# Kernel optimization log

Hardware: AMD Instinct MI355X
Metric: run time of the kernel (lower is better)

The kernel has to match this reference:

```python
import jax, jax.numpy as jnp
import numpy as np

B, I, H, T = 64, 256, 512, 512


def setup_inputs() -> dict:
    key = jax.random.key(0)
    ks = jax.random.split(key, 7)
    x = jax.random.normal(ks[0], (B, I, T), jnp.float32)
    # PyTorch nn.LSTM default init: uniform(-1/sqrt(H), 1/sqrt(H))
    k = 1.0 / np.sqrt(H)
    W_ih = jax.random.uniform(ks[1], (4 * H, I), jnp.float32, -k, k)
    W_hh = jax.random.uniform(ks[2], (4 * H, H), jnp.float32, -k, k)
    b_ih = jax.random.uniform(ks[3], (4 * H,), jnp.float32, -k, k)
    b_hh = jax.random.uniform(ks[4], (4 * H,), jnp.float32, -k, k)
    # init_hidden: xavier_normal_ on zeros(1, B, H) -> N(0, std^2), std = sqrt(2/(fan_in+fan_out))
    # for a (1, B, H) tensor: fan_in = B*H, fan_out = 1*H
    std_h = np.sqrt(2.0 / (B * H + H)).astype(np.float32)
    h0 = std_h * jax.random.normal(ks[5], (B, H), jnp.float32)
    c0 = std_h * jax.random.normal(ks[6], (B, H), jnp.float32)
    return {"x": x, "W_ih": W_ih, "W_hh": W_hh, "b_ih": b_ih, "b_hh": b_hh,
            "h0": h0, "c0": c0}


def _lstm_scan(x, W_ih, W_hh, b_ih, b_hh, h0, c0):
    # x: (B, I, T) -> xs: (T, B, I); precompute input projections for all steps
    xs = jnp.transpose(x, (2, 0, 1))
    gx = jnp.einsum('tbi,gi->tbg', xs, W_ih) + (b_ih + b_hh)  # (T, B, 4H)

    def step(carry, gxt):
        h, c = carry
        gates = gxt + h @ W_hh.T  # (B, 4H)
        i_g, f_g, g_g, o_g = jnp.split(gates, 4, axis=-1)  # PyTorch gate order i,f,g,o
        i_g = jax.nn.sigmoid(i_g)
        f_g = jax.nn.sigmoid(f_g)
        g_g = jnp.tanh(g_g)
        o_g = jax.nn.sigmoid(o_g)
        c_new = f_g * c + i_g * g_g
        h_new = o_g * jnp.tanh(c_new)
        return (h_new, c_new), h_new

    (_, _), hs = jax.lax.scan(step, (h0, c0), gx)  # hs: (T, B, H)
    encoded = jnp.transpose(hs, (1, 2, 0))  # (B, H, T)
    return hs[-1][None], encoded  # mirrors (_, input_encoded)


def reference(x, W_ih, W_hh, b_ih, b_hh, h0, c0):
    return _lstm_scan(x, W_ih, W_hh, b_ih, b_hh, h0, c0)
```

## Files before the change

### kernel.cpp

```cpp
#include <hip/hip_runtime.h>

constexpr int B_ = 64, I_ = 256, H_ = 512, T_ = 512;
constexpr int BH_ = B_ * H_;

constexpr size_t WS_XT_OFF = 524288;

typedef float f32x4 __attribute__((ext_vector_type(4)));
typedef _Float16 h2 __attribute__((ext_vector_type(2)));
typedef _Float16 h8v __attribute__((ext_vector_type(8)));
union H8 { h8v v; h2 p[4]; };

#if defined(__has_builtin)
#if __has_builtin(__builtin_amdgcn_fdot2)
#define HAVE_FDOT2 1
#endif
#endif

__device__ __forceinline__ float dot2(h2 a, h2 b, float c) {
#ifdef HAVE_FDOT2
    return __builtin_amdgcn_fdot2(a, b, c, false);
#else
    return c + (float)a[0] * (float)b[0] + (float)a[1] * (float)b[1];
#endif
}

__device__ __forceinline__ float sigm(float v) { return 1.0f / (1.0f + __expf(-v)); }
__device__ __forceinline__ float tanh_fast(float v) {
    float e = __expf(2.0f * v);
    return 1.0f - 2.0f / (e + 1.0f);
}

__global__ __launch_bounds__(256)
void transpose_x(const float* __restrict__ x, _Float16* __restrict__ xT)
{
    __shared__ float tile[32][33];
    const int b  = blockIdx.z;
    const int i0 = blockIdx.y << 5;
    const int t0 = blockIdx.x << 5;
    const int lt = threadIdx.x;
    const int li = threadIdx.y;
#pragma unroll
    for (int r = 0; r < 4; ++r) {
        int i = li + (r << 3);
        tile[i][lt] = x[((size_t)b * I_ + (i0 + i)) * T_ + (t0 + lt)];
    }
    __syncthreads();
#pragma unroll
    for (int r = 0; r < 4; ++r) {
        int tt = li + (r << 3);
        xT[((size_t)(t0 + tt) * B_ + b) * I_ + (i0 + lt)] = (_Float16)tile[lt][tt];
    }
}

__global__ __launch_bounds__(512, 1)
void lstm_fused(const float* __restrict__ x,
                const _Float16* __restrict__ xT,
                const float* __restrict__ Wih,
                const float* __restrict__ Whh,
                const float* __restrict__ bih,
                const float* __restrict__ bhh,
                const float* __restrict__ h0,
                const float* __restrict__ c0,
                float* __restrict__ out,
                float* __restrict__ hbuf)
{
    __shared__ __align__(16) char smem[47104];
    f32x4* redA  = (f32x4*)smem;
    f32x4* red2  = (f32x4*)smem;
    h2*    actx2 = (h2*)(smem + 34048);
    h2*    acth2 = (h2*)(smem + 34048 + 4224);
    float* hsh   = (float*)(smem + 34048 + 4224 + 8320);

    const int tid  = threadIdx.x;
    const int wv   = tid >> 6;
    const int lane = tid & 63;
    const int jl   = lane & 15;
    const int sl   = wv * 4 + (lane >> 4);

    const int blk = blockIdx.x;
    const int bt  = blk >> 5;
    const int jt  = blk & 31;
    const int b0  = bt << 3;
    const int j0  = jt << 4;

    const int j = j0 + jl;
    h2 wx2[4][4];
    h2 wh2[4][8];
#pragma unroll
    for (int g = 0; g < 4; ++g) {
        const size_t row = (size_t)(g * H_ + j);
#pragma unroll
        for (int q = 0; q < 4; ++q) {
            wx2[g][q][0] = (_Float16)Wih[row * I_ + (sl << 3) + 2 * q];
            wx2[g][q][1] = (_Float16)Wih[row * I_ + (sl << 3) + 2 * q + 1];
        }
#pragma unroll
        for (int q = 0; q < 8; ++q) {
            wh2[g][q][0] = (_Float16)Whh[row * H_ + (sl << 4) + 2 * q];
            wh2[g][q][1] = (_Float16)Whh[row * H_ + (sl << 4) + 2 * q + 1];
        }
    }

    const int fb = b0 + (tid >> 4);
    const int fj = j0 + (tid & 15);
    float c = 0.f;
    f32x4 bias4 = {0.f, 0.f, 0.f, 0.f};
    if (tid < 128) {
        c = c0[(size_t)fb * H_ + fj];
#pragma unroll
        for (int g = 0; g < 4; ++g) bias4[g] = bih[g * H_ + fj] + bhh[g * H_ + fj];
    }

    float* enc = out + BH_;
    const int pr = tid & 127;
    const int qq = tid >> 7;

    const int hs_bq  = jl >> 1;
    const int hs_off = (sl << 4) + ((jl & 1) << 3);
    h2* hdst = acth2 + hs_bq * 260 + (sl << 3) + ((jl & 1) << 2);

    uint2 xv;
    if (xT) xv = *(const uint2*)(xT + (size_t)b0 * I_ + tid * 4);

    for (int t = 0; t < T_; ++t) {
        if (xT) {
            *(uint2*)((char*)(actx2 + (size_t)(tid >> 6) * 132) + (size_t)(tid & 63) * 8) = xv;
        } else {
#pragma unroll
            for (int r = 0; r < 4; ++r) {
                int flat = tid + (r << 9), bb = flat >> 8, ii = flat & 255;
                ((_Float16*)(actx2 + (size_t)bb * 132))[ii] =
                    (_Float16)x[((size_t)(b0 + bb) * I_ + ii) * T_ + t];
            }
        }
        __syncthreads();

        f32x4 v0, v1;
        const float* hsrc = hbuf + (size_t)((t - 1) & 1) * BH_
                          + (size_t)(b0 + hs_bq) * H_ + hs_off;
        if (t > 0) {
            asm volatile("global_load_dwordx4 %0, %2, off sc0 sc1\n\t"
                         "global_load_dwordx4 %1, %3, off sc0 sc1"
                         : "=&v"(v0), "=&v"(v1) : "v"(hsrc), "v"(hsrc + 4));
            __builtin_amdgcn_sched_barrier(0);
        }

        f32x4 r4[8];
#pragma unroll
        for (int bq = 0; bq < 8; ++bq) {
            H8 ax; ax.v = *(const h8v*)(actx2 + (size_t)bq * 132 + (sl << 2));
            float s0 = 0.f, s1 = 0.f, s2 = 0.f, s3 = 0.f;
#pragma unroll
            for (int q = 0; q < 4; ++q) {
                s0 = dot2(ax.p[q], wx2[0][q], s0);
                s1 = dot2(ax.p[q], wx2[1][q], s1);
                s2 = dot2(ax.p[q], wx2[2][q], s2);
                s3 = dot2(ax.p[q], wx2[3][q], s3);
            }
            r4[bq] = (f32x4){s0, s1, s2, s3};
        }

        if (t > 0) {
            asm volatile("s_waitcnt vmcnt(0)" ::: "memory");
            __builtin_amdgcn_sched_barrier(0);
            const float Kc = 2.0f + 2.0f * (float)(((t - 1) >> 1) & 1);
            bool ok = true;
#pragma unroll
            for (int e = 0; e < 4; ++e) {
                ok = ok && (fabsf(v0[e] - Kc) < 0.75f);
                ok = ok && (fabsf(v1[e] - Kc) < 0.75f);
            }
            for (unsigned it = 0; !ok && it < 32768u; ++it) {
                __builtin_amdgcn_s_sleep(1);
                asm volatile("global_load_dwordx4 %0, %2, off sc0 sc1\n\t"
                             "global_load_dwordx4 %1, %3, off sc0 sc1\n\t"
                             "s_waitcnt vmcnt(0)"
                             : "=&v"(v0), "=&v"(v1) : "v"(hsrc), "v"(hsrc + 4) : "memory");
                ok = true;
#pragma unroll
                for (int e = 0; e < 4; ++e) {
                    ok = ok && (fabsf(v0[e] - Kc) < 0.75f);
                    ok = ok && (fabsf(v1[e] - Kc) < 0.75f);
                }
            }
            v0 = (v0 - Kc) * 2.0f;
            v1 = (v1 - Kc) * 2.0f;
        } else {
            const float* src = h0 + (size_t)(b0 + hs_bq) * H_ + hs_off;
            v0 = *(const f32x4*)src;
            v1 = *(const f32x4*)(src + 4);
        }
        {
            H8 hv;
#pragma unroll
            for (int e = 0; e < 2; ++e) { hv.p[e][0]   = (_Float16)v0[2*e];
                                          hv.p[e][1]   = (_Float16)v0[2*e+1];
                                          hv.p[e+2][0] = (_Float16)v1[2*e];
                                          hv.p[e+2][1] = (_Float16)v1[2*e+1]; }
            *(h8v*)hdst = hv.v;
            asm volatile("s_waitcnt lgkmcnt(0)" ::: "memory");
            __builtin_amdgcn_sched_barrier(0);
        }

        if (xT && t + 1 < T_)
            xv = *(const uint2*)(xT + ((size_t)(t + 1) * B_ + b0) * I_ + tid * 4);

#pragma unroll
        for (int bq = 0; bq < 8; ++bq) {
            H8 a0, a1;
            a0.v = *(const h8v*)(acth2 + (size_t)bq * 260 + (sl << 3));
            a1.v = *(const h8v*)(acth2 + (size_t)bq * 260 + (sl << 3) + 4);
            float s0 = r4[bq][0], s1 = r4[bq][1], s2 = r4[bq][2], s3 = r4[bq][3];
#pragma unroll
            for (int q = 0; q < 4; ++q) {
                s0 = dot2(a0.p[q], wh2[0][q], s0);
                s1 = dot2(a0.p[q], wh2[1][q], s1);
                s2 = dot2(a0.p[q], wh2[2][q], s2);
                s3 = dot2(a0.p[q], wh2[3][q], s3);
            }
#pragma unroll
            for (int q = 0; q < 4; ++q) {
                s0 = dot2(a1.p[q], wh2[0][q + 4], s0);
                s1 = dot2(a1.p[q], wh2[1][q + 4], s1);
                s2 = dot2(a1.p[q], wh2[2][q + 4], s2);
                s3 = dot2(a1.p[q], wh2[3][q + 4], s3);
            }
            r4[bq] = (f32x4){s0, s1, s2, s3};
        }

        if (wv < 4) {
#pragma unroll
            for (int bq = 0; bq < 8; ++bq) redA[sl * 133 + bq * 16 + jl] = r4[bq];
        }
        __syncthreads();
        f32x4 acc = redA[(qq * 4 + 0) * 133 + pr] + redA[(qq * 4 + 1) * 133 + pr]
                  + redA[(qq * 4 + 2) * 133 + pr] + redA[(qq * 4 + 3) * 133 + pr];
        __syncthreads();
        if (wv >= 4) {
#pragma unroll
            for (int bq = 0; bq < 8; ++bq) redA[(sl - 16) * 133 + bq * 16 + jl] = r4[bq];
        }
        __syncthreads();
        acc += redA[(qq * 4 + 0) * 133 + pr] + redA[(qq * 4 + 1) * 133 + pr]
             + redA[(qq * 4 + 2) * 133 + pr] + redA[(qq * 4 + 3) * 133 + pr];
        __syncthreads();
        red2[qq * 133 + pr] = acc;
        __syncthreads();

        if (tid < 128) {
            f32x4 G = red2[0 * 133 + tid] + red2[1 * 133 + tid]
                    + red2[2 * 133 + tid] + red2[3 * 133 + tid] + bias4;
            float ig = sigm(G[0]), fg = sigm(G[1]);
            float gg = tanh_fast(G[2]);
            float og = sigm(G[3]);
            c = fg * c + ig * gg;
            float hv = og * tanh_fast(c);
            hsh[tid] = hv;
            enc[((size_t)fb * H_ + fj) * T_ + t] = hv;
            if (t == T_ - 1) out[(size_t)fb * H_ + fj] = hv;
        }

        if (t != T_ - 1) {
            __syncthreads();
            if (tid < 32) {
                const float Kp = 2.0f + 2.0f * (float)((t >> 1) & 1);
                int bq = tid >> 2, q4 = tid & 3;
                f32x4 v = *(const f32x4*)(hsh + bq * 16 + q4 * 4);
                v = v * 0.5f + Kp;
                float* dst = hbuf + (size_t)(t & 1) * BH_
                           + (size_t)(b0 + bq) * H_ + j0 + q4 * 4;
                asm volatile("global_store_dwordx4 %0, %1, off sc0 sc1"
                             :: "v"(dst), "v"(v) : "memory");
            }
        }
    }
}

extern "C" void kernel_launch(void* const* d_in, const int* in_sizes, int n_in,
                              void* d_out, int out_size, void* d_ws, size_t ws_size,
                              hipStream_t stream)
{
    (void)in_sizes; (void)n_in; (void)out_size;
    const float* x   = (const float*)d_in[0];
    const float* Wih = (const float*)d_in[1];
    const float* Whh = (const float*)d_in[2];
    const float* bih = (const float*)d_in[3];
    const float* bhh = (const float*)d_in[4];
    const float* h0  = (const float*)d_in[5];
    const float* c0  = (const float*)d_in[6];
    float* out  = (float*)d_out;
    float* hbuf = (float*)d_ws;

    const size_t xt_bytes = (size_t)T_ * B_ * I_ * sizeof(_Float16);
    _Float16* xT = nullptr;
    if (ws_size >= WS_XT_OFF + xt_bytes)
        xT = (_Float16*)((char*)d_ws + WS_XT_OFF);

    hipMemsetAsync(d_ws, 0, 2 * BH_ * sizeof(float), stream);
    if (xT)
        transpose_x<<<dim3(T_ / 32, I_ / 32, B_), dim3(32, 8), 0, stream>>>(x, xT);

    void* args[] = { (void*)&x, (void*)&xT, (void*)&Wih, (void*)&Whh, (void*)&bih,
                     (void*)&bhh, (void*)&h0, (void*)&c0, (void*)&out, (void*)&hbuf };
    hipLaunchCooperativeKernel((void*)lstm_fused, dim3(256), dim3(512), args, 0, stream);
}
```

Measured before the change: 1.827 ms.

## Split waves across batch halves to cut reduction barriers in LSTM step

Reorganizes the per-block work so each group of four waves handles half the batch rows with twice the reduction depth per thread, doubling register-held weight slices. The partial sums now go to shared memory in a single pass, replacing the multi-stage reduction that used five block barriers per step. The hidden-state publish is done within each wave after a local LDS wait, removing another block barrier. In exchange it uses more VGPRs for weights and has a longer serial 16-way sum in the gate threads.

```diff
diff --git a/kernel.cpp b/kernel.cpp
--- a/kernel.cpp
+++ b/kernel.cpp
@@ -64,18 +64,19 @@
                 float* __restrict__ out,
                 float* __restrict__ hbuf)
 {
-    __shared__ __align__(16) char smem[47104];
+    __shared__ __align__(16) char smem[47232];
     f32x4* redA  = (f32x4*)smem;
-    f32x4* red2  = (f32x4*)smem;
     h2*    actx2 = (h2*)(smem + 34048);
     h2*    acth2 = (h2*)(smem + 34048 + 4224);
-    float* hsh   = (float*)(smem + 34048 + 4224 + 8320);
+    float* hsh   = (float*)(smem + 34048 + 4224 + 8448);
 
     const int tid  = threadIdx.x;
     const int wv   = tid >> 6;
     const int lane = tid & 63;
     const int jl   = lane & 15;
-    const int sl   = wv * 4 + (lane >> 4);
+    const int slq  = lane >> 4;
+    const int bg   = wv >> 2;
+    const int sl16 = ((wv & 3) << 2) | slq;
 
     const int blk = blockIdx.x;
     const int bt  = blk >> 5;
@@ -84,20 +85,20 @@
     const int j0  = jt << 4;
 
     const int j = j0 + jl;
-    h2 wx2[4][4];
-    h2 wh2[4][8];
+    h2 wx2[4][8];
+    h2 wh2[4][16];
 #pragma unroll
     for (int g = 0; g < 4; ++g) {
         const size_t row = (size_t)(g * H_ + j);
 #pragma unroll
-        for (int q = 0; q < 4; ++q) {
-            wx2[g][q][0] = (_Float16)Wih[row * I_ + (sl << 3) + 2 * q];
-            wx2[g][q][1] = (_Float16)Wih[row * I_ + (sl << 3) + 2 * q + 1];
-        }
-#pragma unroll
         for (int q = 0; q < 8; ++q) {
-            wh2[g][q][0] = (_Float16)Whh[row * H_ + (sl << 4) + 2 * q];
-            wh2[g][q][1] = (_Float16)Whh[row * H_ + (sl << 4) + 2 * q + 1];
+            wx2[g][q][0] = (_Float16)Wih[row * I_ + (sl16 << 4) + 2 * q];
+            wx2[g][q][1] = (_Float16)Wih[row * I_ + (sl16 << 4) + 2 * q + 1];
+        }
+#pragma unroll
+        for (int q = 0; q < 16; ++q) {
+            wh2[g][q][0] = (_Float16)Whh[row * H_ + (sl16 << 5) + 2 * q];
+            wh2[g][q][1] = (_Float16)Whh[row * H_ + (sl16 << 5) + 2 * q + 1];
         }
     }
 
@@ -112,12 +113,10 @@
     }
 
     float* enc = out + BH_;
-    const int pr = tid & 127;
-    const int qq = tid >> 7;
-
-    const int hs_bq  = jl >> 1;
-    const int hs_off = (sl << 4) + ((jl & 1) << 3);
-    h2* hdst = acth2 + hs_bq * 260 + (sl << 3) + ((jl & 1) << 2);
+
+    const int sb     = (bg << 2) + (lane >> 4);
+    const int hb_off = ((wv & 3) << 7) + ((lane & 15) << 3);
+    h2* hdst = acth2 + sb * 264 + (hb_off >> 1);
 
     uint2 xv;
     if (xT) xv = *(const uint2*)(xT + (size_t)b0 * I_ + tid * 4);
@@ -137,7 +136,7 @@
 
         f32x4 v0, v1;
         const float* hsrc = hbuf + (size_t)((t - 1) & 1) * BH_
-                          + (size_t)(b0 + hs_bq) * H_ + hs_off;
+                          + (size_t)(b0 + sb) * H_ + hb_off;
         if (t > 0) {
             asm volatile("global_load_dwordx4 %0, %2, off sc0 sc1\n\t"
                          "global_load_dwordx4 %1, %3, off sc0 sc1"
@@ -145,19 +144,29 @@
             __builtin_amdgcn_sched_barrier(0);
         }
 
-        f32x4 r4[8];
-#pragma unroll
-        for (int bq = 0; bq < 8; ++bq) {
-            H8 ax; ax.v = *(const h8v*)(actx2 + (size_t)bq * 132 + (sl << 2));
+        f32x4 r4[4];
+#pragma unroll
+        for (int i = 0; i < 4; ++i) {
+            const int bq = (bg << 2) + i;
+            H8 ax0, ax1;
+            ax0.v = *(const h8v*)(actx2 + (size_t)bq * 132 + (sl16 << 3));
+            ax1.v = *(const h8v*)(actx2 + (size_t)bq * 132 + (sl16 << 3) + 4);
             float s0 = 0.f, s1 = 0.f, s2 = 0.f, s3 = 0.f;
 #pragma unroll
             for (int q = 0; q < 4; ++q) {
-                s0 = dot2(ax.p[q], wx2[0][q], s0);
-                s1 = dot2(ax.p[q], wx2[1][q], s1);
-                s2 = dot2(ax.p[q], wx2[2][q], s2);
-                s3 = dot2(ax.p[q], wx2[3][q], s3);
-            }
-            r4[bq] = (f32x4){s0, s1, s2, s3};
+                s0 = dot2(ax0.p[q], wx2[0][q], s0);
+                s1 = dot2(ax0.p[q], wx2[1][q], s1);
+                s2 = dot2(ax0.p[q], wx2[2][q], s2);
+                s3 = dot2(ax0.p[q], wx2[3][q], s3);
+            }
+#pragma unroll
+            for (int q = 0; q < 4; ++q) {
+                s0 = dot2(ax1.p[q], wx2[0][q + 4], s0);
+                s1 = dot2(ax1.p[q], wx2[1][q + 4], s1);
+                s2 = dot2(ax1.p[q], wx2[2][q + 4], s2);
+                s3 = dot2(ax1.p[q], wx2[3][q + 4], s3);
+            }
+            r4[i] = (f32x4){s0, s1, s2, s3};
         }
 
         if (t > 0) {
@@ -186,7 +195,7 @@
             v0 = (v0 - Kc) * 2.0f;
             v1 = (v1 - Kc) * 2.0f;
         } else {
-            const float* src = h0 + (size_t)(b0 + hs_bq) * H_ + hs_off;
+            const float* src = h0 + (size_t)(b0 + sb) * H_ + hb_off;
             v0 = *(const f32x4*)src;
             v1 = *(const f32x4*)(src + 4);
         }
@@ -206,11 +215,15 @@
             xv = *(const uint2*)(xT + ((size_t)(t + 1) * B_ + b0) * I_ + tid * 4);
 
 #pragma unroll
-        for (int bq = 0; bq < 8; ++bq) {
-            H8 a0, a1;
-            a0.v = *(const h8v*)(acth2 + (size_t)bq * 260 + (sl << 3));
-            a1.v = *(const h8v*)(acth2 + (size_t)bq * 260 + (sl << 3) + 4);
-            float s0 = r4[bq][0], s1 = r4[bq][1], s2 = r4[bq][2], s3 = r4[bq][3];
+        for (int i = 0; i < 4; ++i) {
+            const int bq = (bg << 2) + i;
+            const h2* hrow = acth2 + (size_t)bq * 264 + (sl16 << 4);
+            H8 a0, a1, a2, a3;
+            a0.v = *(const h8v*)(hrow);
+            a1.v = *(const h8v*)(hrow + 4);
+            a2.v = *(const h8v*)(hrow + 8);
+            a3.v = *(const h8v*)(hrow + 12);
+            float s0 = r4[i][0], s1 = r4[i][1], s2 = r4[i][2], s3 = r4[i][3];
 #pragma unroll
             for (int q = 0; q < 4; ++q) {
                 s0 = dot2(a0.p[q], wh2[0][q], s0);
@@ -225,31 +238,32 @@
                 s2 = dot2(a1.p[q], wh2[2][q + 4], s2);
                 s3 = dot2(a1.p[q], wh2[3][q + 4], s3);
             }
-            r4[bq] = (f32x4){s0, s1, s2, s3};
-        }
-
-        if (wv < 4) {
-#pragma unroll
-            for (int bq = 0; bq < 8; ++bq) redA[sl * 133 + bq * 16 + jl] = r4[bq];
-        }
+#pragma unroll
+            for (int q = 0; q < 4; ++q) {
+                s0 = dot2(a2.p[q], wh2[0][q + 8], s0);
+                s1 = dot2(a2.p[q], wh2[1][q + 8], s1);
+                s2 = dot2(a2.p[q], wh2[2][q + 8], s2);
+                s3 = dot2(a2.p[q], wh2[3][q + 8], s3);
+            }
+#pragma unroll
+            for (int q = 0; q < 4; ++q) {
+                s0 = dot2(a3.p[q], wh2[0][q + 12], s0);
+                s1 = dot2(a3.p[q], wh2[1][q + 12], s1);
+                s2 = dot2(a3.p[q], wh2[2][q + 12], s2);
+                s3 = dot2(a3.p[q], wh2[3][q + 12], s3);
+            }
+            r4[i] = (f32x4){s0, s1, s2, s3};
+        }
+
+#pragma unroll
+        for (int i = 0; i < 4; ++i)
+            redA[sl16 * 133 + (((bg << 2) + i) << 4) + jl] = r4[i];
         __syncthreads();
-        f32x4 acc = redA[(qq * 4 + 0) * 133 + pr] + redA[(qq * 4 + 1) * 133 + pr]
-                  + redA[(qq * 4 + 2) * 133 + pr] + redA[(qq * 4 + 3) * 133 + pr];
-        __syncthreads();
-        if (wv >= 4) {
-#pragma unroll
-            for (int bq = 0; bq < 8; ++bq) redA[(sl - 16) * 133 + bq * 16 + jl] = r4[bq];
-        }
-        __syncthreads();
-        acc += redA[(qq * 4 + 0) * 133 + pr] + redA[(qq * 4 + 1) * 133 + pr]
-             + redA[(qq * 4 + 2) * 133 + pr] + redA[(qq * 4 + 3) * 133 + pr];
-        __syncthreads();
-        red2[qq * 133 + pr] = acc;
-        __syncthreads();
 
         if (tid < 128) {
-            f32x4 G = red2[0 * 133 + tid] + red2[1 * 133 + tid]
-                    + red2[2 * 133 + tid] + red2[3 * 133 + tid] + bias4;
+            f32x4 G = bias4;
+#pragma unroll
+            for (int s = 0; s < 16; ++s) G += redA[s * 133 + tid];
             float ig = sigm(G[0]), fg = sigm(G[1]);
             float gg = tanh_fast(G[2]);
             float og = sigm(G[3]);
@@ -257,20 +271,21 @@
             float hv = og * tanh_fast(c);
             hsh[tid] = hv;
             enc[((size_t)fb * H_ + fj) * T_ + t] = hv;
-            if (t == T_ - 1) out[(size_t)fb * H_ + fj] = hv;
-        }
-
-        if (t != T_ - 1) {
-            __syncthreads();
-            if (tid < 32) {
-                const float Kp = 2.0f + 2.0f * (float)((t >> 1) & 1);
-                int bq = tid >> 2, q4 = tid & 3;
-                f32x4 v = *(const f32x4*)(hsh + bq * 16 + q4 * 4);
-                v = v * 0.5f + Kp;
-                float* dst = hbuf + (size_t)(t & 1) * BH_
-                           + (size_t)(b0 + bq) * H_ + j0 + q4 * 4;
-                asm volatile("global_store_dwordx4 %0, %1, off sc0 sc1"
-                             :: "v"(dst), "v"(v) : "memory");
+            if (t == T_ - 1) {
+                out[(size_t)fb * H_ + fj] = hv;
+            } else {
+                asm volatile("s_waitcnt lgkmcnt(0)" ::: "memory");
+                __builtin_amdgcn_sched_barrier(0);
+                if (lane < 16) {
+                    const float Kp = 2.0f + 2.0f * (float)((t >> 1) & 1);
+                    f32x4 v = *(const f32x4*)(&hsh[(wv << 6) + ((lane >> 2) << 4) + ((lane & 3) << 2)]);
+                    v = v * 0.5f + Kp;
+                    float* dst = hbuf + (size_t)(t & 1) * BH_
+                               + (size_t)(b0 + (wv << 2) + (lane >> 2)) * H_
+                               + j0 + ((lane & 3) << 2);
+                    asm volatile("global_store_dwordx4 %0, %1, off sc0 sc1"
+                                 :: "v"(dst), "v"(v) : "memory");
+                }
             }
         }
     }
```

Measured after the change: 1.652 ms (median of 2 runs). 1.11x faster.
